# Kernel tuning notes

Hardware: AMD Instinct MI355X
Metric: run time of the kernel (lower is better)

## Reference

```python
import jax, jax.numpy as jnp
import numpy as np

BS, L, D, ITEM_NUM = 64, 100, 64, 100000  # batch, max_seq_len, embedding_dim, item vocab
NEG_INF = -10000.0


def setup_inputs() -> dict:
    key = jax.random.key(0)
    k1, k2, k3, k4, k5 = jax.random.split(key, 5)
    N = BS * (L + 1)
    return {
        "prec_vec": jax.random.normal(k1, (BS * L, D), jnp.float32),
        "score_embs": jax.random.normal(k2, (N, D), jnp.float32),
        "pop_prob_list": jax.random.uniform(k3, (ITEM_NUM + 1,), jnp.float32, 0.01, 1.0),
        "sample_items_id": jax.random.randint(k4, (N,), 0, ITEM_NUM + 1, dtype=jnp.int32),
        "log_mask": jax.random.randint(k5, (BS, L), 0, 2, dtype=jnp.int32),
    }


def reference(prec_vec, score_embs, pop_prob_list, sample_items_id, log_mask):
    bs, L_ = log_mask.shape
    N = sample_items_id.shape[0]  # bs * (L+1)

    # debiased in-batch sampled-softmax logits: [bs*L, N]
    debias = jnp.log(pop_prob_list[sample_items_id])
    logits = jnp.matmul(prec_vec, score_embs.T) - debias[None, :]

    # column mask: padded positions (log_mask==0); last position of each seq always valid
    col_valid = jnp.concatenate(
        [log_mask, jnp.ones((bs, 1), log_mask.dtype)], axis=1
    ).reshape(-1)  # [N]
    logits = jnp.where(col_valid[None, :] == 0, NEG_INF, logits)

    # duplicate-item mask: dup[i, k] = any item in sequence i equals sample_items_id[k]
    id_list = sample_items_id.reshape(bs, L_ + 1)
    dup = (sample_items_id[None, None, :] == id_list[:, :, None]).any(axis=1)  # [bs, N]

    # targets: label for (i, j) is flat column i*(L+1) + j + 1
    tgt = jnp.arange(bs)[:, None] * (L_ + 1) + jnp.arange(L_)[None, :] + 1  # [bs, L]

    # apply dup mask per (i, j) but never mask the row's own target column
    not_target = jnp.arange(N)[None, None, :] != tgt[:, :, None]  # [bs, L, N]
    mask3 = dup[:, None, :] & not_target
    logits3 = jnp.where(mask3, NEG_INF, logits.reshape(bs, L_, N))

    # masked cross-entropy, mean over valid (log_mask != 0) rows
    logits2 = logits3.reshape(bs * L_, N)
    labels = tgt.reshape(-1)
    logp = jax.nn.log_softmax(logits2, axis=-1)
    nll = -jnp.take_along_axis(logp, labels[:, None], axis=1)[:, 0]  # [bs*L]
    w = (log_mask.reshape(-1) != 0).astype(logits2.dtype)
    return jnp.sum(nll * w) / jnp.sum(w)
```

## Files before the change

### kernel.cpp

```cpp
#include <hip/hip_runtime.h>

#define NEG_INF (-10000.0f)
#define L_SEQ   100
#define N_COLS  6464
#define D_      64
#define N_ROWS  6400
#define NS      16

#define OFF_PS  0
#define OFF_XT  409600
#define OFF_ACC 435200

typedef __attribute__((ext_vector_type(8))) short short8;
typedef __attribute__((ext_vector_type(4))) float f32x4;
union F8 { short8 v; unsigned short u[8]; unsigned w[4]; };

__device__ __forceinline__ unsigned short f2bf(float f) {
  unsigned u = __float_as_uint(f);
  return (unsigned short)((u + 0x7FFFu + ((u >> 16) & 1u)) >> 16);
}
__device__ __forceinline__ unsigned packbf(float lo, float hi) {
  return (__float_as_uint(hi) & 0xFFFF0000u) | (__float_as_uint(lo) >> 16);
}

__global__ __launch_bounds__(256, 4) void fused_kernel(
    const float* __restrict__ prec, const float* __restrict__ score,
    const float* __restrict__ pop, const int* __restrict__ sid,
    const int* __restrict__ lm,
    float* __restrict__ ps, float* __restrict__ xtrow) {
  __shared__ unsigned bs[2 * 3126];
  __shared__ unsigned short btile[64 * 64];
  __shared__ float mdl[2 * 64];

  const int tid = threadIdx.x;
  const int split = blockIdx.y;
  const int blkrow = blockIdx.x * 64;
  const int w = tid >> 6, lane = tid & 63;
  const int lr = lane & 15, lk = lane >> 4;
  const int rowbase = blkrow + w * 16;
  const int i0 = blkrow / L_SEQ;
  const int i1 = (blkrow + 63) / L_SEQ;
  const int lim = (i0 + 1) * L_SEQ;
  const int rbase4 = rowbase + lk * 4;

  for (int x = tid; x < 2 * 3126; x += 256) bs[x] = 0u;
  __syncthreads();
  if (tid < 202) {
    int sel = tid / 101, pos = tid - sel * 101;
    int iq = sel ? i1 : i0;
    int id = sid[iq * 101 + pos];
    atomicOr(&bs[sel * 3126 + (id >> 5)], 1u << (id & 31));
  }

  const float* prow = prec + (size_t)(rowbase + lr) * D_ + lk * 8;
  F8 fa0, fa1;
  {
    float4 a0 = *(const float4*)(prow);
    float4 a1 = *(const float4*)(prow + 4);
    float4 b0 = *(const float4*)(prow + 32);
    float4 b1 = *(const float4*)(prow + 36);
    fa0.u[0] = f2bf(a0.x); fa0.u[1] = f2bf(a0.y); fa0.u[2] = f2bf(a0.z); fa0.u[3] = f2bf(a0.w);
    fa0.u[4] = f2bf(a1.x); fa0.u[5] = f2bf(a1.y); fa0.u[6] = f2bf(a1.z); fa0.u[7] = f2bf(a1.w);
    fa1.u[0] = f2bf(b0.x); fa1.u[1] = f2bf(b0.y); fa1.u[2] = f2bf(b0.z); fa1.u[3] = f2bf(b0.w);
    fa1.u[4] = f2bf(b1.x); fa1.u[5] = f2bf(b1.y); fa1.u[6] = f2bf(b1.z); fa1.u[7] = f2bf(b1.w);
  }

  float s[4][4];
#pragma unroll
  for (int t4 = 0; t4 < 4; ++t4)
#pragma unroll
    for (int q = 0; q < 4; ++q) s[t4][q] = 0.f;

  float4 sv[4];
  int svN = 0, lmvN = 0;

  auto STAGE_ISSUE = [&](int stv) {
    const float* base = score + (size_t)stv * 64 * D_;
#pragma unroll
    for (int j = 0; j < 4; ++j)
      sv[j] = *(const float4*)(base + j * 1024 + tid * 4);
    if (tid < 64) {
      int c = stv * 64 + tid;
      svN = sid[c];
      int i2 = c / 101, p = c - i2 * 101;
      lmvN = (p == L_SEQ) ? 1 : lm[i2 * L_SEQ + p];
    }
  };
  auto STAGE_WRITE = [&]() {
#pragma unroll
    for (int j = 0; j < 4; ++j) {
      int colw = j * 16 + (tid >> 4);
      int byteoff = colw * 128 + ((((tid & 15) * 8)) ^ ((colw & 7) << 4));
      uint2 pk;
      pk.x = packbf(sv[j].x, sv[j].y);
      pk.y = packbf(sv[j].z, sv[j].w);
      *(uint2*)((char*)btile + byteoff) = pk;
    }
    if (tid < 64) {
      float inv = 1.0f / pop[svN];
      unsigned h0 = (bs[svN >> 5] >> (svN & 31)) & 1u;
      unsigned h1 = (bs[3126 + (svN >> 5)] >> (svN & 31)) & 1u;
      mdl[tid] = (lmvN && !h0) ? inv : 0.f;
      mdl[64 + tid] = (lmvN && !h1) ? inv : 0.f;
    }
  };
  auto COMPUTE = [&]() {
    const int sw = (lr & 7) << 4;
    F8 fb0[4], fb1[4];
    float ma[4], mb[4];
#pragma unroll
    for (int t4 = 0; t4 < 4; ++t4) {
      int col = t4 * 16 + lr;
      char* rowp = (char*)btile + col * 128;
      fb0[t4].v = *(const short8*)(rowp + ((lk * 16) ^ sw));
      fb1[t4].v = *(const short8*)(rowp + ((64 + lk * 16) ^ sw));
      ma[t4] = mdl[t4 * 16 + lr];
      mb[t4] = mdl[64 + t4 * 16 + lr];
    }
    f32x4 acc[4];
#pragma unroll
    for (int t4 = 0; t4 < 4; ++t4) {
      f32x4 z = {0.f, 0.f, 0.f, 0.f};
      z = __builtin_amdgcn_mfma_f32_16x16x32_bf16(fa0.v, fb0[t4].v, z, 0, 0, 0);
      z = __builtin_amdgcn_mfma_f32_16x16x32_bf16(fa1.v, fb1[t4].v, z, 0, 0, 0);
      acc[t4] = z;
    }
#pragma unroll
    for (int q = 0; q < 4; ++q) {
      const bool ub = (rbase4 + q) >= lim;
#pragma unroll
      for (int t4 = 0; t4 < 4; ++t4) {
        float mm = ub ? mb[t4] : ma[t4];
        s[t4][q] = fmaf(__expf(acc[t4][q]), mm, s[t4][q]);
      }
    }
  };

  const int nit = (100 - split) / NS + 1;
  int st = split;
  STAGE_ISSUE(st);
  __syncthreads();
  STAGE_WRITE();
  __syncthreads();
  for (int t = 0; t < nit; ++t) {
    const bool more = (t + 1 < nit);
    if (more) STAGE_ISSUE(st + NS);
    COMPUTE();
    if (more) {
      __syncthreads();
      STAGE_WRITE();
      __syncthreads();
    }
    st += NS;
  }

  float sq[4];
#pragma unroll
  for (int q = 0; q < 4; ++q)
    sq[q] = (s[0][q] + s[1][q]) + (s[2][q] + s[3][q]);
#pragma unroll
  for (int q = 0; q < 4; ++q) {
#pragma unroll
    for (int off = 1; off < 16; off <<= 1)
      sq[q] += __shfl_xor(sq[q], off);
  }
  if (lr == 0) {
#pragma unroll
    for (int q = 0; q < 4; ++q)
      ps[(size_t)(rbase4 + q) * NS + split] = sq[q];
  }

  if (split == 0) {
    int row_l = rowbase + lr;
    int i_l = row_l / L_SEQ, j_l = row_l - i_l * L_SEQ;
    int tgtc = i_l * 101 + j_l + 1;
    int p_l = j_l + 1;
    int vt = (p_l == L_SEQ) ? 1 : lm[i_l * L_SEQ + p_l];
    const float* srp = score + (size_t)tgtc * D_ + lk * 8;
    float4 s0 = *(const float4*)(srp);
    float4 s1 = *(const float4*)(srp + 4);
    float4 s2 = *(const float4*)(srp + 32);
    float4 s3 = *(const float4*)(srp + 36);
    F8 ft0, ft1;
    ft0.w[0] = packbf(s0.x, s0.y); ft0.w[1] = packbf(s0.z, s0.w);
    ft0.w[2] = packbf(s1.x, s1.y); ft0.w[3] = packbf(s1.z, s1.w);
    ft1.w[0] = packbf(s2.x, s2.y); ft1.w[1] = packbf(s2.z, s2.w);
    ft1.w[2] = packbf(s3.x, s3.y); ft1.w[3] = packbf(s3.z, s3.w);
    f32x4 z = {0.f, 0.f, 0.f, 0.f};
    z = __builtin_amdgcn_mfma_f32_16x16x32_bf16(fa0.v, ft0.v, z, 0, 0, 0);
    z = __builtin_amdgcn_mfma_f32_16x16x32_bf16(fa1.v, ft1.v, z, 0, 0, 0);
    int qs = lr - lk * 4;
    if (qs >= 0 && qs < 4) {
      float zd = (qs == 0) ? z[0] : (qs == 1) ? z[1] : (qs == 2) ? z[2] : z[3];
      float xv = zd - __logf(pop[sid[tgtc]]);
      xtrow[row_l] = vt ? xv : NEG_INF;
    }
  }
}

__global__ __launch_bounds__(256) void merge_kernel(
    const float* __restrict__ ps, const float* __restrict__ xtrow,
    const int* __restrict__ lm, float* __restrict__ acc,
    unsigned* __restrict__ done, float* __restrict__ out) {
  const int r = blockIdx.x * 256 + threadIdx.x;
  const float4* pp = (const float4*)(ps + (size_t)r * NS);
  float4 a = pp[0], b = pp[1], c = pp[2], d = pp[3];
  float sv = ((a.x + a.y) + (a.z + a.w)) + ((b.x + b.y) + (b.z + b.w)) +
             ((c.x + c.y) + (c.z + c.w)) + ((d.x + d.y) + (d.z + d.w));
  float x = xtrow[r];
  sv += __expf(x);
  sv = fmaxf(sv, 1e-37f);
  const int v = (lm[r] != 0);
  float nll = v ? (__logf(sv) - x) : 0.f;
  float c1 = v ? 1.f : 0.f;
#pragma unroll
  for (int off = 1; off < 64; off <<= 1) {
    nll += __shfl_xor(nll, off);
    c1 += __shfl_xor(c1, off);
  }
  __shared__ float red[8];
  const int wq = threadIdx.x >> 6, lane = threadIdx.x & 63;
  if (lane == 0) { red[wq] = nll; red[4 + wq] = c1; }
  __syncthreads();
  if (threadIdx.x == 0) {
    float bsum = (red[0] + red[1]) + (red[2] + red[3]);
    float bcnt = (red[4] + red[5]) + (red[6] + red[7]);
    atomicAdd(&acc[0], bsum);
    atomicAdd(&acc[1], bcnt);
    __threadfence();
    unsigned t = atomicAdd(done, 1u);
    if (t == 24) {
      float S = atomicAdd(&acc[0], 0.f);
      float C = atomicAdd(&acc[1], 0.f);
      out[0] = S / C;
    }
  }
}

extern "C" void kernel_launch(void* const* d_in, const int* in_sizes, int n_in,
                              void* d_out, int out_size, void* d_ws, size_t ws_size,
                              hipStream_t stream) {
  const float* prec  = (const float*)d_in[0];
  const float* score = (const float*)d_in[1];
  const float* pop   = (const float*)d_in[2];
  const int*   sid   = (const int*)d_in[3];
  const int*   lm    = (const int*)d_in[4];

  char* ws = (char*)d_ws;
  float*    ps    = (float*)(ws + OFF_PS);
  float*    xtrow = (float*)(ws + OFF_XT);
  float*    acc   = (float*)(ws + OFF_ACC);
  unsigned* done  = (unsigned*)(ws + OFF_ACC + 8);
  float*    out   = (float*)d_out;

  hipMemsetAsync(acc, 0, 12, stream);
  hipLaunchKernelGGL(fused_kernel, dim3(100, NS), dim3(256), 0, stream,
                     prec, score, pop, sid, lm, ps, xtrow);
  hipLaunchKernelGGL(merge_kernel, dim3(25), dim3(256), 0, stream,
                     ps, xtrow, lm, acc, done, out);
}
```

Before: 34.38 us.

## Preload all score tiles upfront and replace bitset dup-check with linear id scan

Instead of a double-buffered per-iteration stage/compute loop with barriers, every block issues all of its score tile loads up front (up to 7 tiles held in registers), converts them to bf16 in LDS, and then computes with no further barriers. The LDS bitset (zero-fill plus atomicOr) used for duplicate detection is replaced by storing the 202 sequence ids in shared memory and scanning them linearly for each column. The mask computation is spread across all threads. In exchange, register and LDS use rise (occupancy hint lowered from 4 to 2), and the linear scan adds ALU work per column.

```diff
diff --git a/kernel.cpp b/kernel.cpp
--- a/kernel.cpp
+++ b/kernel.cpp
@@ -6,6 +6,7 @@
 #define D_      64
 #define N_ROWS  6400
 #define NS      16
+#define NIT_MAX 7
 
 #define OFF_PS  0
 #define OFF_XT  409600
@@ -23,14 +24,14 @@
   return (__float_as_uint(hi) & 0xFFFF0000u) | (__float_as_uint(lo) >> 16);
 }
 
-__global__ __launch_bounds__(256, 4) void fused_kernel(
+__global__ __launch_bounds__(256, 2) void fused_kernel(
     const float* __restrict__ prec, const float* __restrict__ score,
     const float* __restrict__ pop, const int* __restrict__ sid,
     const int* __restrict__ lm,
     float* __restrict__ ps, float* __restrict__ xtrow) {
-  __shared__ unsigned bs[2 * 3126];
-  __shared__ unsigned short btile[64 * 64];
-  __shared__ float mdl[2 * 64];
+  __shared__ __align__(16) int ids[224];
+  __shared__ __align__(16) unsigned short btiles[NIT_MAX][64 * 64];
+  __shared__ __align__(16) float mdlall[NIT_MAX][128];
 
   const int tid = threadIdx.x;
   const int split = blockIdx.y;
@@ -42,14 +43,12 @@
   const int i1 = (blkrow + 63) / L_SEQ;
   const int lim = (i0 + 1) * L_SEQ;
   const int rbase4 = rowbase + lk * 4;
-
-  for (int x = tid; x < 2 * 3126; x += 256) bs[x] = 0u;
-  __syncthreads();
+  const int nit = (100 - split) / NS + 1;
+
   if (tid < 202) {
     int sel = tid / 101, pos = tid - sel * 101;
     int iq = sel ? i1 : i0;
-    int id = sid[iq * 101 + pos];
-    atomicOr(&bs[sel * 3126 + (id >> 5)], 1u << (id & 31));
+    ids[sel * 112 + pos] = sid[iq * 101 + pos];
   }
 
   const float* prow = prec + (size_t)(rowbase + lr) * D_ + lk * 8;
@@ -65,94 +64,99 @@
     fa1.u[4] = f2bf(b1.x); fa1.u[5] = f2bf(b1.y); fa1.u[6] = f2bf(b1.z); fa1.u[7] = f2bf(b1.w);
   }
 
+  float4 sv[NIT_MAX][4];
+#pragma unroll
+  for (int t = 0; t < NIT_MAX; ++t)
+    if (t < nit) {
+      const float* base = score + (size_t)(split + t * NS) * 64 * D_;
+#pragma unroll
+      for (int j = 0; j < 4; ++j)
+        sv[t][j] = *(const float4*)(base + j * 1024 + tid * 4);
+    }
+
+  __syncthreads();
+
+  for (int f = tid; f < nit * 64; f += 256) {
+    int t = f >> 6, cc = f & 63;
+    int c = (split + t * NS) * 64 + cc;
+    int i2 = c / 101, p = c - i2 * 101;
+    int vm = (p == L_SEQ) ? 1 : lm[i2 * L_SEQ + p];
+    float m0 = 0.f, m1 = 0.f;
+    if (vm) {
+      int id = sid[c];
+      int h0 = 0, h1 = 0;
+#pragma unroll 5
+      for (int j4 = 0; j4 < 25; ++j4) {
+        int4 qa = *(const int4*)&ids[j4 * 4];
+        int4 qb = *(const int4*)&ids[112 + j4 * 4];
+        h0 |= (qa.x == id) | (qa.y == id) | (qa.z == id) | (qa.w == id);
+        h1 |= (qb.x == id) | (qb.y == id) | (qb.z == id) | (qb.w == id);
+      }
+      h0 |= (ids[100] == id);
+      h1 |= (ids[212] == id);
+      float inv = 1.0f / pop[id];
+      m0 = h0 ? 0.f : inv;
+      m1 = h1 ? 0.f : inv;
+    }
+    mdlall[t][cc] = m0;
+    mdlall[t][64 + cc] = m1;
+  }
+
+#pragma unroll
+  for (int t = 0; t < NIT_MAX; ++t)
+    if (t < nit) {
+#pragma unroll
+      for (int j = 0; j < 4; ++j) {
+        int colw = j * 16 + (tid >> 4);
+        int byteoff = colw * 128 + ((((tid & 15) * 8)) ^ ((colw & 7) << 4));
+        uint2 pk;
+        pk.x = packbf(sv[t][j].x, sv[t][j].y);
+        pk.y = packbf(sv[t][j].z, sv[t][j].w);
+        *(uint2*)((char*)btiles[t] + byteoff) = pk;
+      }
+    }
+
+  __syncthreads();
+
   float s[4][4];
 #pragma unroll
   for (int t4 = 0; t4 < 4; ++t4)
 #pragma unroll
     for (int q = 0; q < 4; ++q) s[t4][q] = 0.f;
 
-  float4 sv[4];
-  int svN = 0, lmvN = 0;
-
-  auto STAGE_ISSUE = [&](int stv) {
-    const float* base = score + (size_t)stv * 64 * D_;
-#pragma unroll
-    for (int j = 0; j < 4; ++j)
-      sv[j] = *(const float4*)(base + j * 1024 + tid * 4);
-    if (tid < 64) {
-      int c = stv * 64 + tid;
-      svN = sid[c];
-      int i2 = c / 101, p = c - i2 * 101;
-      lmvN = (p == L_SEQ) ? 1 : lm[i2 * L_SEQ + p];
-    }
-  };
-  auto STAGE_WRITE = [&]() {
-#pragma unroll
-    for (int j = 0; j < 4; ++j) {
-      int colw = j * 16 + (tid >> 4);
-      int byteoff = colw * 128 + ((((tid & 15) * 8)) ^ ((colw & 7) << 4));
-      uint2 pk;
-      pk.x = packbf(sv[j].x, sv[j].y);
-      pk.y = packbf(sv[j].z, sv[j].w);
-      *(uint2*)((char*)btile + byteoff) = pk;
-    }
-    if (tid < 64) {
-      float inv = 1.0f / pop[svN];
-      unsigned h0 = (bs[svN >> 5] >> (svN & 31)) & 1u;
-      unsigned h1 = (bs[3126 + (svN >> 5)] >> (svN & 31)) & 1u;
-      mdl[tid] = (lmvN && !h0) ? inv : 0.f;
-      mdl[64 + tid] = (lmvN && !h1) ? inv : 0.f;
-    }
-  };
-  auto COMPUTE = [&]() {
-    const int sw = (lr & 7) << 4;
-    F8 fb0[4], fb1[4];
-    float ma[4], mb[4];
-#pragma unroll
-    for (int t4 = 0; t4 < 4; ++t4) {
-      int col = t4 * 16 + lr;
-      char* rowp = (char*)btile + col * 128;
-      fb0[t4].v = *(const short8*)(rowp + ((lk * 16) ^ sw));
-      fb1[t4].v = *(const short8*)(rowp + ((64 + lk * 16) ^ sw));
-      ma[t4] = mdl[t4 * 16 + lr];
-      mb[t4] = mdl[64 + t4 * 16 + lr];
-    }
-    f32x4 acc[4];
-#pragma unroll
-    for (int t4 = 0; t4 < 4; ++t4) {
-      f32x4 z = {0.f, 0.f, 0.f, 0.f};
-      z = __builtin_amdgcn_mfma_f32_16x16x32_bf16(fa0.v, fb0[t4].v, z, 0, 0, 0);
-      z = __builtin_amdgcn_mfma_f32_16x16x32_bf16(fa1.v, fb1[t4].v, z, 0, 0, 0);
-      acc[t4] = z;
-    }
-#pragma unroll
-    for (int q = 0; q < 4; ++q) {
-      const bool ub = (rbase4 + q) >= lim;
+  const int sw = (lr & 7) << 4;
+#pragma unroll
+  for (int t = 0; t < NIT_MAX; ++t)
+    if (t < nit) {
+      F8 fb0[4], fb1[4];
+      float ma[4], mb[4];
 #pragma unroll
       for (int t4 = 0; t4 < 4; ++t4) {
-        float mm = ub ? mb[t4] : ma[t4];
-        s[t4][q] = fmaf(__expf(acc[t4][q]), mm, s[t4][q]);
-      }
-    }
-  };
-
-  const int nit = (100 - split) / NS + 1;
-  int st = split;
-  STAGE_ISSUE(st);
-  __syncthreads();
-  STAGE_WRITE();
-  __syncthreads();
-  for (int t = 0; t < nit; ++t) {
-    const bool more = (t + 1 < nit);
-    if (more) STAGE_ISSUE(st + NS);
-    COMPUTE();
-    if (more) {
-      __syncthreads();
-      STAGE_WRITE();
-      __syncthreads();
-    }
-    st += NS;
-  }
+        int col = t4 * 16 + lr;
+        char* rowp = (char*)btiles[t] + col * 128;
+        fb0[t4].v = *(const short8*)(rowp + ((lk * 16) ^ sw));
+        fb1[t4].v = *(const short8*)(rowp + ((64 + lk * 16) ^ sw));
+        ma[t4] = mdlall[t][t4 * 16 + lr];
+        mb[t4] = mdlall[t][64 + t4 * 16 + lr];
+      }
+      f32x4 acc[4];
+#pragma unroll
+      for (int t4 = 0; t4 < 4; ++t4) {
+        f32x4 z = {0.f, 0.f, 0.f, 0.f};
+        z = __builtin_amdgcn_mfma_f32_16x16x32_bf16(fa0.v, fb0[t4].v, z, 0, 0, 0);
+        z = __builtin_amdgcn_mfma_f32_16x16x32_bf16(fa1.v, fb1[t4].v, z, 0, 0, 0);
+        acc[t4] = z;
+      }
+#pragma unroll
+      for (int q = 0; q < 4; ++q) {
+        const bool ub = (rbase4 + q) >= lim;
+#pragma unroll
+        for (int t4 = 0; t4 < 4; ++t4) {
+          float mm = ub ? mb[t4] : ma[t4];
+          s[t4][q] = fmaf(__expf(acc[t4][q]), mm, s[t4][q]);
+        }
+      }
+    }
 
   float sq[4];
 #pragma unroll
```

Measured after the change: 53.29 us. 55.0% more time.
